# Performance work log

Measured on AMD Instinct MI355X. Metric: run time of the kernel, lower is better.

## Reference

```python
import jax, jax.numpy as jnp
import numpy as np

B, S, D, H, DK = 8, 1024, 1024, 16, 64
DV = D // H  # 64


def setup_inputs() -> dict:
    key = jax.random.key(0)
    ks = jax.random.split(key, 9)
    s = 1.0 / np.sqrt(D)
    return {
        "x": jax.random.normal(ks[0], (B, S, D), dtype=jnp.float32),
        "masks": jnp.ones((B, S), dtype=jnp.int32),
        "Wq": jax.random.normal(ks[1], (D, H * DK), dtype=jnp.float32) * s,
        "bq": jnp.zeros((H * DK,), dtype=jnp.float32),
        "Wk": jax.random.normal(ks[2], (D, H * DK), dtype=jnp.float32) * s,
        "bk": jnp.zeros((H * DK,), dtype=jnp.float32),
        "Wv": jax.random.normal(ks[3], (D, H * DV), dtype=jnp.float32) * s,
        "bv": jnp.zeros((H * DV,), dtype=jnp.float32),
        "Wo": jax.random.normal(ks[4], (H * DV, D), dtype=jnp.float32) * s,
        "bo": jnpp_zeros() if False else jnp.zeros((D,), dtype=jnp.float32),
    }


def reference(x, masks, Wq, bq, Wk, bk, Wv, bv, Wo, bo):
    # projections -> [B, H, S, d]
    q = (x @ Wq + bq).reshape(B, S, H, DK).transpose(0, 2, 1, 3)
    k = (x @ Wk + bk).reshape(B, S, H, DK).transpose(0, 2, 1, 3)
    v = (x @ Wv + bv).reshape(B, S, H, DV).transpose(0, 2, 1, 3)
    # scaled dot-product attention with padding mask
    logits = jnp.einsum('bhqd,bhkd->bhqk', q, k) / jnp.sqrt(jnp.float32(DK))
    mask = masks[:, None, None, :]  # [B,1,1,S]
    logits = jnp.where(mask == 0, jnp.float32(-1e9), logits)
    scores = jax.nn.softmax(logits, axis=-1)
    out = jnp.einsum('bhqk,bhkd->bhqd', scores, v)
    out = out.transpose(0, 2, 1, 3).reshape(B, S, H * DV)
    # output projection; dropout is identity in eval mode
    return out @ Wo + bo
```

## Files before the change

### kernel.cpp

```cpp
#include <hip/hip_runtime.h>
#include <stdint.h>

#define B_ 8
#define S_ 1024
#define D_ 1024
#define H_ 16
#define DK_ 64
#define DV_ 64

typedef __attribute__((ext_vector_type(8))) short short8;
typedef __attribute__((ext_vector_type(4))) float f32x4;

__device__ __forceinline__ unsigned short f2bf(float f) {
  union { float f; unsigned u; } v; v.f = f;
  return (unsigned short)((v.u + 0x7fffu + ((v.u >> 16) & 1u)) >> 16);
}
__device__ __forceinline__ unsigned short f2bf_trunc(float f) {
  union { float f; unsigned u; } v; v.f = f;
  return (unsigned short)(v.u >> 16);
}

__device__ __forceinline__ void ld_lds16(const unsigned short* g, unsigned short* l) {
  __builtin_amdgcn_global_load_lds((const __attribute__((address_space(1))) void*)g,
                                   (__attribute__((address_space(3))) void*)l, 16, 0, 0);
}

__global__ __launch_bounds__(256) void prep_kernel(const float* __restrict__ x,
                                                   unsigned short* __restrict__ xb,
                                                   const float* __restrict__ W0,
                                                   const float* __restrict__ W1,
                                                   const float* __restrict__ W2,
                                                   const float* __restrict__ W3,
                                                   unsigned short* __restrict__ T0,
                                                   unsigned short* __restrict__ T1,
                                                   unsigned short* __restrict__ T2,
                                                   unsigned short* __restrict__ T3) {
  const int z = blockIdx.z;
  if (z >= 4) {
    size_t blk = (size_t)(z - 4) * 256 + blockIdx.y * 16 + blockIdx.x;
    size_t i = (blk * 256 + threadIdx.x) * 4;
    float4 v = *(const float4*)(x + i);
    ushort4 o;
    o.x = f2bf(v.x); o.y = f2bf(v.y); o.z = f2bf(v.z); o.w = f2bf(v.w);
    *(ushort4*)(xb + i) = o;
    return;
  }
  __shared__ __align__(16) unsigned short tl[64][65];
  const float* W; unsigned short* Wt;
  switch (z) {
    case 0: W = W0; Wt = T0; break;
    case 1: W = W1; Wt = T1; break;
    case 2: W = W2; Wt = T2; break;
    default: W = W3; Wt = T3; break;
  }
  const int xx = threadIdx.x & 63;
  const int y4 = threadIdx.x >> 6;
  const int bn = blockIdx.x * 64;
  const int bk = blockIdx.y * 64;
  #pragma unroll
  for (int r = y4; r < 64; r += 4)
    tl[r][xx] = f2bf(W[(size_t)(bk + r) * 1024 + bn + xx]);
  __syncthreads();
  #pragma unroll
  for (int r = y4; r < 64; r += 4)
    Wt[(size_t)(bn + r) * 1024 + bk + xx] = tl[xx][r];
}


struct SJob { const unsigned short* g; unsigned short* l; };

__device__ __forceinline__ void stage128(const unsigned short* __restrict__ G,
                                         unsigned short* __restrict__ L, int t) {
  #pragma unroll
  for (int i = 0; i < 2; i++) {
    int s = i * 512 + t;
    int r = s >> 3, cb = s & 7;
    int c = cb ^ (r & 7);
    ld_lds16(G + (size_t)r * 1024 + c * 8, L + (size_t)s * 8);
  }
}

template <bool SW>
__device__ __forceinline__ f32x4 MM(short8 a, short8 b, f32x4 c) {
  if constexpr (SW) return __builtin_amdgcn_mfma_f32_16x16x32_bf16(b, a, c, 0, 0, 0);
  else              return __builtin_amdgcn_mfma_f32_16x16x32_bf16(a, b, c, 0, 0, 0);
}

template <bool SW, int VM>
__device__ __forceinline__ void ktile2(const unsigned short* __restrict__ As_,
                                       const unsigned short* __restrict__ Bs_,
                                       f32x4 (&acc)[4][4],
                                       SJob a0, SJob a1, SJob b2,
                                       int t, int wm, int wn, int l15, int quad, int l7) {
  const int cb0 = (quad ^ l7) * 8;
  const int cb1 = ((4 | quad) ^ l7) * 8;
  short8 af[4], bf[4];

  #pragma unroll
  for (int mi = 0; mi < 4; mi++)
    af[mi] = *(const short8*)&As_[(wm + mi * 16 + l15) * 64 + cb0];
  #pragma unroll
  for (int ni = 0; ni < 4; ni++)
    bf[ni] = *(const short8*)&Bs_[(wn + ni * 16 + l15) * 64 + cb0];
  if (a0.g) stage128(a0.g, a0.l, t);
  if (a1.g) stage128(a1.g, a1.l, t);
  if (b2.g) stage128(b2.g, b2.l, t);
  __builtin_amdgcn_s_barrier();
  asm volatile("s_waitcnt lgkmcnt(0)" ::: "memory");
  __builtin_amdgcn_s_setprio(1);
  #pragma unroll
  for (int mi = 0; mi < 4; mi++)
    #pragma unroll
    for (int ni = 0; ni < 4; ni++)
      acc[mi][ni] = MM<SW>(af[mi], bf[ni], acc[mi][ni]);
  __builtin_amdgcn_s_setprio(0);
  __builtin_amdgcn_s_barrier();

  #pragma unroll
  for (int mi = 0; mi < 4; mi++)
    af[mi] = *(const short8*)&As_[(wm + mi * 16 + l15) * 64 + cb1];
  #pragma unroll
  for (int ni = 0; ni < 4; ni++)
    bf[ni] = *(const short8*)&Bs_[(wn + ni * 16 + l15) * 64 + cb1];
  __builtin_amdgcn_s_barrier();
  asm volatile("s_waitcnt lgkmcnt(0)" ::: "memory");
  __builtin_amdgcn_s_setprio(1);
  #pragma unroll
  for (int mi = 0; mi < 4; mi++)
    #pragma unroll
    for (int ni = 0; ni < 4; ni++)
      acc[mi][ni] = MM<SW>(af[mi], bf[ni], acc[mi][ni]);
  __builtin_amdgcn_s_setprio(0);
  if constexpr (VM >= 0) {
    if constexpr (VM == 2) asm volatile("s_waitcnt vmcnt(2)" ::: "memory");
    else                   asm volatile("s_waitcnt vmcnt(0)" ::: "memory");
  }
  __builtin_amdgcn_s_barrier();
}

template <bool SW>
__device__ __forceinline__ void gemm_core(const unsigned short* __restrict__ Ag,
                                          const unsigned short* __restrict__ Bg,
                                          unsigned short* __restrict__ Asl,
                                          unsigned short* __restrict__ Bsl,
                                          f32x4 (&acc)[4][4],
                                          int t, int wm, int wn, int l15, int quad, int l7) {
  stage128(Ag, &Asl[0], t);
  stage128(Ag + 128 * 1024, &Asl[8192], t);
  stage128(Bg, &Bsl[0], t);
  stage128(Bg + 64, &Bsl[8192], t);
  asm volatile("s_waitcnt vmcnt(2)" ::: "memory");
  __builtin_amdgcn_s_barrier();

  #pragma unroll 1
  for (int Jb = 0; Jb < 12; Jb += 6) {
    const unsigned short* Agj = Ag + (size_t)Jb * 64;
    const unsigned short* Bgj = Bg + (size_t)Jb * 64;
    ktile2<SW, 2>(&Asl[0], &Bsl[0], acc,
                  SJob{Agj + 64, &Asl[16384]}, SJob{Agj + 64 + 128 * 1024, &Asl[16384 + 8192]},
                  SJob{Bgj + 128, &Bsl[16384]}, t, wm, wn, l15, quad, l7);
    ktile2<SW, 2>(&Asl[16384], &Bsl[8192], acc,
                  SJob{Agj + 128, &Asl[0]}, SJob{Agj + 128 + 128 * 1024, &Asl[8192]},
                  SJob{Bgj + 192, &Bsl[0]}, t, wm, wn, l15, quad, l7);
    ktile2<SW, 2>(&Asl[0], &Bsl[16384], acc,
                  SJob{Agj + 192, &Asl[16384]}, SJob{Agj + 192 + 128 * 1024, &Asl[16384 + 8192]},
                  SJob{Bgj + 256, &Bsl[8192]}, t, wm, wn, l15, quad, l7);
    ktile2<SW, 2>(&Asl[16384], &Bsl[0], acc,
                  SJob{Agj + 256, &Asl[0]}, SJob{Agj + 256 + 128 * 1024, &Asl[8192]},
                  SJob{Bgj + 320, &Bsl[16384]}, t, wm, wn, l15, quad, l7);
    ktile2<SW, 2>(&Asl[0], &Bsl[8192], acc,
                  SJob{Agj + 320, &Asl[16384]}, SJob{Agj + 320 + 128 * 1024, &Asl[16384 + 8192]},
                  SJob{Bgj + 384, &Bsl[0]}, t, wm, wn, l15, quad, l7);
    ktile2<SW, 2>(&Asl[16384], &Bsl[16384], acc,
                  SJob{Agj + 384, &Asl[0]}, SJob{Agj + 384 + 128 * 1024, &Asl[8192]},
                  SJob{Bgj + 448, &Bsl[8192]}, t, wm, wn, l15, quad, l7);
  }
  ktile2<SW, 2>(&Asl[0], &Bsl[0], acc,
                SJob{Ag + 13 * 64, &Asl[16384]}, SJob{Ag + 13 * 64 + 128 * 1024, &Asl[16384 + 8192]},
                SJob{Bg + 14 * 64, &Bsl[16384]}, t, wm, wn, l15, quad, l7);
  ktile2<SW, 2>(&Asl[16384], &Bsl[8192], acc,
                SJob{Ag + 14 * 64, &Asl[0]}, SJob{Ag + 14 * 64 + 128 * 1024, &Asl[8192]},
                SJob{Bg + 15 * 64, &Bsl[0]}, t, wm, wn, l15, quad, l7);
  ktile2<SW, 0>(&Asl[0], &Bsl[16384], acc,
                SJob{Ag + 15 * 64, &Asl[16384]}, SJob{Ag + 15 * 64 + 128 * 1024, &Asl[16384 + 8192]},
                SJob{nullptr, nullptr}, t, wm, wn, l15, quad, l7);
  ktile2<SW, -1>(&Asl[16384], &Bsl[0], acc,
                 SJob{nullptr, nullptr}, SJob{nullptr, nullptr}, SJob{nullptr, nullptr},
                 t, wm, wn, l15, quad, l7);
}

__global__ __launch_bounds__(512, 2) void gemm_qkv8(const unsigned short* __restrict__ A,
                                                    const unsigned short* __restrict__ Bt,
                                                    const float* __restrict__ bq,
                                                    const float* __restrict__ bk,
                                                    const float* __restrict__ bv,
                                                    const int* __restrict__ masks,
                                                    unsigned short* __restrict__ q,
                                                    unsigned short* __restrict__ kk,
                                                    unsigned short* __restrict__ vT) {
  extern __shared__ unsigned short lds[];
  unsigned short* Asl = lds;
  unsigned short* Bsl = lds + 2 * 16384;
  const int t = threadIdx.x;
  const int w = t >> 6, lane = t & 63;
  const int l15 = lane & 15, quad = lane >> 4, l7 = l15 & 7;
  const int bm = blockIdx.y * 256, bn = blockIdx.x * 128;
  const int wm = (w >> 1) * 64, wn = (w & 1) * 64;
  const bool vsec = (blockIdx.x >= 16);
  const unsigned short* Ag = A + (size_t)bm * 1024;
  const unsigned short* Bg = Bt + (size_t)bn * 1024;

  f32x4 acc[4][4] = {};
  if (!vsec) gemm_core<false>(Ag, Bg, Asl, Bsl, acc, t, wm, wn, l15, quad, l7);
  else       gemm_core<true >(Ag, Bg, Asl, Bsl, acc, t, wm, wn, l15, quad, l7);

  if (!vsec) {
    int sec = blockIdx.x >> 3;
    const float* bsel = (sec == 0) ? bq : bk;
    unsigned short* dst = (sec == 0) ? q : kk;
    float scale = (sec == 0) ? 0.180336880f : 1.0f;
    #pragma unroll
    for (int ni = 0; ni < 4; ni++) {
      int c = (bn & 1023) + wn + ni * 16 + l15;
      float bvv = bsel[c];
      int hh = c >> 6, d = c & 63;
      #pragma unroll
      for (int mi = 0; mi < 4; mi++) {
        int row0 = bm + wm + mi * 16 + quad * 4;
        #pragma unroll
        for (int r = 0; r < 4; r++) {
          int row = row0 + r;
          int b = row >> 10, s = row & 1023;
          dst[(((size_t)(b * H_ + hh)) * S_ + s) * DK_ + d] = f2bf((acc[mi][ni][r] + bvv) * scale);
        }
      }
    }
  } else {
    #pragma unroll
    for (int ni = 0; ni < 4; ni++) {
      int cbase = (bn & 1023) + wn + ni * 16;
      #pragma unroll
      for (int mi = 0; mi < 4; mi++) {
        int row = bm + wm + mi * 16 + l15;
        int b = row >> 10, s = row & 1023;
        float mf = (masks[b * S_ + s] != 0) ? 1.0f : 0.0f;
        #pragma unroll
        for (int r = 0; r < 4; r++) {
          int c = cbase + quad * 4 + r;
          int hh = c >> 6, d = c & 63;
          vT[(((size_t)(b * H_ + hh)) * DV_ + d) * S_ + s] = f2bf((acc[mi][ni][r] + bv[c]) * mf);
        }
      }
    }
  }
}

__global__ __launch_bounds__(512, 2) void gemm_out8(const unsigned short* __restrict__ A,
                                                    const unsigned short* __restrict__ Bt,
                                                    const float* __restrict__ bias,
                                                    float* __restrict__ Cout) {
  extern __shared__ unsigned short lds[];
  unsigned short* Asl = lds;
  unsigned short* Bsl = lds + 2 * 16384;
  const int t = threadIdx.x;
  const int w = t >> 6, lane = t & 63;
  const int l15 = lane & 15, quad = lane >> 4, l7 = l15 & 7;
  const int bm = blockIdx.y * 256, bn = blockIdx.x * 128;
  const int wm = (w >> 1) * 64, wn = (w & 1) * 64;
  const unsigned short* Ag = A + (size_t)bm * 1024;
  const unsigned short* Bg = Bt + (size_t)bn * 1024;

  f32x4 acc[4][4] = {};
  gemm_core<false>(Ag, Bg, Asl, Bsl, acc, t, wm, wn, l15, quad, l7);

  #pragma unroll
  for (int ni = 0; ni < 4; ni++) {
    int col = bn + wn + ni * 16 + l15;
    float bvv = bias[col];
    #pragma unroll
    for (int mi = 0; mi < 4; mi++) {
      int row0 = bm + wm + mi * 16 + quad * 4;
      #pragma unroll
      for (int r = 0; r < 4; r++)
        Cout[(size_t)(row0 + r) * 1024 + col] = acc[mi][ni][r] + bvv;
    }
  }
}

#define PLD 72
#define VROWS 65
__global__ __launch_bounds__(256) void attn_kernel(const unsigned short* __restrict__ Q,
                                                   const unsigned short* __restrict__ Kb,
                                                   const unsigned short* __restrict__ Vt,
                                                   const int* __restrict__ masks,
                                                   unsigned short* __restrict__ O) {
  __shared__ __align__(16) unsigned short Pl[128 * PLD];
  __shared__ __align__(16) unsigned short Ks[2 * 64 * 64];
  __shared__ __align__(16) unsigned short Vs[(2 * VROWS + 15) * 64];
  const int t = threadIdx.x;
  const int wave = t >> 6, lane = t & 63;
  const int l15 = lane & 15, quad = lane >> 4;
  const int l7 = l15 & 7;
  const int bh = blockIdx.x;
  const int qt = blockIdx.y;
  const int b = bh >> 4, h = bh & 15;

  const unsigned short* Qg = Q + ((size_t)bh * S_ + qt * 128) * DK_;
  const unsigned short* Kg = Kb + (size_t)bh * S_ * DK_;
  const unsigned short* Vg = Vt + (size_t)bh * DV_ * S_;
  const int wslot = (t & ~63);

  int mv[4];
  #pragma unroll
  for (int j = 0; j < 4; j++)
    mv[j] = masks[b * S_ + (j * 4 + wave) * 64 + lane];

  short8 aq[2][2];
  #pragma unroll
  for (int mb = 0; mb < 2; mb++)
    #pragma unroll
    for (int kf = 0; kf < 2; kf++)
      aq[mb][kf] = *(const short8*)(Qg + (size_t)(wave * 32 + mb * 16 + l15) * 64 + kf * 32 + quad * 8);

  auto stage = [&](int kt, int buf) {
    const unsigned short* Kt = Kg + (size_t)kt * 64 * DK_;
    unsigned short* Kd = &Ks[buf * 4096];
    unsigned short* Vd = &Vs[buf * (VROWS * 64)];
    #pragma unroll
    for (int i = 0; i < 2; i++) {
      int p = i * 256 + t;
      int rk = p >> 3, ck = (p & 7) ^ (rk & 7);
      ld_lds16(Kt + (size_t)rk * DK_ + ck * 8, &Kd[(i * 256 + wslot) * 8]);
      ld_lds16(Vg + (size_t)rk * S_ + kt * 64 + ck * 8, &Vd[(i * 256 + wslot) * 8]);
    }
    if (wave == (kt & 3))
      Vd[64 * 64 + lane] = (mv[kt >> 2] != 0) ? (unsigned short)0x3F80 : (unsigned short)0;
  };

  f32x4 o_acc[2][5] = {};

  stage(0, 0);
  __syncthreads();

  #pragma unroll 2
  for (int kt = 0; kt < 16; kt++) {
    const int cur = kt & 1;
    if (kt < 15) stage(kt + 1, cur ^ 1);
    const unsigned short* Kc = &Ks[cur * 4096];
    const unsigned short* Vc = &Vs[cur * (VROWS * 64)];

    f32x4 sc[2][4];
    #pragma unroll
    for (int n = 0; n < 4; n++) {
      short8 bk0 = *(const short8*)&Kc[(n * 16 + l15) * 64 + (quad ^ l7) * 8];
      short8 bk1 = *(const short8*)&Kc[(n * 16 + l15) * 64 + ((4 + quad) ^ l7) * 8];
      #pragma unroll
      for (int mb = 0; mb < 2; mb++) {
        f32x4 c = {};
        c = __builtin_amdgcn_mfma_f32_16x16x32_bf16(bk0, aq[mb][0], c, 0, 0, 0);
        c = __builtin_amdgcn_mfma_f32_16x16x32_bf16(bk1, aq[mb][1], c, 0, 0, 0);
        sc[mb][n] = c;
      }
    }
    #pragma unroll
    for (int mb = 0; mb < 2; mb++)
      #pragma unroll
      for (int n = 0; n < 4; n++) {
        ushort4 pk;
        pk.x = f2bf_trunc(__builtin_amdgcn_exp2f(sc[mb][n][0]));
        pk.y = f2bf_trunc(__builtin_amdgcn_exp2f(sc[mb][n][1]));
        pk.z = f2bf_trunc(__builtin_amdgcn_exp2f(sc[mb][n][2]));
        pk.w = f2bf_trunc(__builtin_amdgcn_exp2f(sc[mb][n][3]));
        *(ushort4*)&Pl[(wave * 32 + mb * 16 + l15) * PLD + n * 16 + quad * 4] = pk;
      }
    #pragma unroll
    for (int kf = 0; kf < 2; kf++) {
      short8 ap[2];
      #pragma unroll
      for (int mb = 0; mb < 2; mb++)
        ap[mb] = *(const short8*)&Pl[(wave * 32 + mb * 16 + l15) * PLD + kf * 32 + quad * 8];
      #pragma unroll
      for (int n = 0; n < 5; n++) {
        short8 bv = *(const short8*)&Vc[(n * 16 + l15) * 64 + ((kf * 4 + quad) ^ l7) * 8];
        #pragma unroll
        for (int mb = 0; mb < 2; mb++)
          o_acc[mb][n] = __builtin_amdgcn_mfma_f32_16x16x32_bf16(ap[mb], bv, o_acc[mb][n], 0, 0, 0);
      }
    }
    __syncthreads();
  }

  #pragma unroll
  for (int mb = 0; mb < 2; mb++)
    #pragma unroll
    for (int r = 0; r < 4; r++) {
      float l = __shfl(o_acc[mb][4][r], lane & 48, 64);
      float inv = __builtin_amdgcn_rcpf(l);
      int qrow = qt * 128 + wave * 32 + mb * 16 + quad * 4 + r;
      #pragma unroll
      for (int n = 0; n < 4; n++) {
        int col = h * 64 + n * 16 + l15;
        O[((size_t)b * S_ + qrow) * D_ + col] = f2bf(o_acc[mb][n][r] * inv);
      }
    }
}

extern "C" void kernel_launch(void* const* d_in, const int* in_sizes, int n_in,
                              void* d_out, int out_size, void* d_ws, size_t ws_size,
                              hipStream_t stream) {
  (void)in_sizes; (void)n_in; (void)out_size; (void)ws_size;
  const float* x  = (const float*)d_in[0];
  const int* masks = (const int*)d_in[1];
  const float* Wq = (const float*)d_in[2];
  const float* bq = (const float*)d_in[3];
  const float* Wk = (const float*)d_in[4];
  const float* bk = (const float*)d_in[5];
  const float* Wv = (const float*)d_in[6];
  const float* bv = (const float*)d_in[7];
  const float* Wo = (const float*)d_in[8];
  const float* bo = (const float*)d_in[9];

  char* p = (char*)d_ws;
  unsigned short* xb    = (unsigned short*)p; p += (size_t)8192 * 1024 * 2;
  unsigned short* WqkvT = (unsigned short*)p; p += (size_t)3072 * 1024 * 2;
  unsigned short* WoT   = (unsigned short*)p; p += (size_t)1024 * 1024 * 2;
  unsigned short* q     = (unsigned short*)p; p += (size_t)8192 * 1024 * 2;
  unsigned short* kk    = (unsigned short*)p; p += (size_t)8192 * 1024 * 2;
  unsigned short* vT    = (unsigned short*)p; p += (size_t)8192 * 1024 * 2;
  unsigned short* at    = (unsigned short*)p; p += (size_t)8192 * 1024 * 2;

  static bool attr_done = false;
  if (!attr_done) {
    hipFuncSetAttribute((const void*)gemm_qkv8, hipFuncAttributeMaxDynamicSharedMemorySize, 114688);
    hipFuncSetAttribute((const void*)gemm_out8, hipFuncAttributeMaxDynamicSharedMemorySize, 114688);
    attr_done = true;
  }

  prep_kernel<<<dim3(16, 16, 36), 256, 0, stream>>>(
      x, xb, Wq, Wk, Wv, Wo,
      WqkvT, WqkvT + (size_t)1024 * 1024, WqkvT + (size_t)2048 * 1024, WoT);
  gemm_qkv8<<<dim3(24, 32), 512, 114688, stream>>>(xb, WqkvT, bq, bk, bv, masks, q, kk, vT);
  attn_kernel<<<dim3(128, 8), 256, 0, stream>>>(q, kk, vT, masks, at);
  gemm_out8<<<dim3(8, 32), 512, 114688, stream>>>(at, WoT, bo, (float*)d_out);
}
```

Before: 251.2 us.

## Triple-buffer GEMM LDS pipeline and remap blocks across XCDs

Restructures the shared GEMM core from double to triple LDS buffering, prefetching two k-tiles ahead and waiting on vmcnt(6) instead of vmcnt(2). The B-tile load is issued after the first half-tile of MFMAs rather than together with the A loads. Both GEMM kernels also remap linear block IDs so that consecutive blocks land on different XCDs, aiming for better L2 locality. Dynamic LDS rises to 144 KB per block, which constrains occupancy.

```diff
diff --git a/kernel.cpp b/kernel.cpp
--- a/kernel.cpp
+++ b/kernel.cpp
@@ -104,6 +104,23 @@
     bf[ni] = *(const short8*)&Bs_[(wn + ni * 16 + l15) * 64 + cb0];
   if (a0.g) stage128(a0.g, a0.l, t);
   if (a1.g) stage128(a1.g, a1.l, t);
+  __builtin_amdgcn_s_barrier();
+  asm volatile("s_waitcnt lgkmcnt(0)" ::: "memory");
+  __builtin_amdgcn_s_setprio(1);
+  #pragma unroll
+  for (int mi = 0; mi < 4; mi++)
+    #pragma unroll
+    for (int ni = 0; ni < 4; ni++)
+      acc[mi][ni] = MM<SW>(af[mi], bf[ni], acc[mi][ni]);
+  __builtin_amdgcn_s_setprio(0);
+  __builtin_amdgcn_s_barrier();
+
+  #pragma unroll
+  for (int mi = 0; mi < 4; mi++)
+    af[mi] = *(const short8*)&As_[(wm + mi * 16 + l15) * 64 + cb1];
+  #pragma unroll
+  for (int ni = 0; ni < 4; ni++)
+    bf[ni] = *(const short8*)&Bs_[(wn + ni * 16 + l15) * 64 + cb1];
   if (b2.g) stage128(b2.g, b2.l, t);
   __builtin_amdgcn_s_barrier();
   asm volatile("s_waitcnt lgkmcnt(0)" ::: "memory");
@@ -114,27 +131,8 @@
     for (int ni = 0; ni < 4; ni++)
       acc[mi][ni] = MM<SW>(af[mi], bf[ni], acc[mi][ni]);
   __builtin_amdgcn_s_setprio(0);
-  __builtin_amdgcn_s_barrier();
-
-  #pragma unroll
-  for (int mi = 0; mi < 4; mi++)
-    af[mi] = *(const short8*)&As_[(wm + mi * 16 + l15) * 64 + cb1];
-  #pragma unroll
-  for (int ni = 0; ni < 4; ni++)
-    bf[ni] = *(const short8*)&Bs_[(wn + ni * 16 + l15) * 64 + cb1];
-  __builtin_amdgcn_s_barrier();
-  asm volatile("s_waitcnt lgkmcnt(0)" ::: "memory");
-  __builtin_amdgcn_s_setprio(1);
-  #pragma unroll
-  for (int mi = 0; mi < 4; mi++)
-    #pragma unroll
-    for (int ni = 0; ni < 4; ni++)
-      acc[mi][ni] = MM<SW>(af[mi], bf[ni], acc[mi][ni]);
-  __builtin_amdgcn_s_setprio(0);
-  if constexpr (VM >= 0) {
-    if constexpr (VM == 2) asm volatile("s_waitcnt vmcnt(2)" ::: "memory");
-    else                   asm volatile("s_waitcnt vmcnt(0)" ::: "memory");
-  }
+  if constexpr (VM == 6) asm volatile("s_waitcnt vmcnt(6)" ::: "memory");
+  if constexpr (VM == 0) asm volatile("s_waitcnt vmcnt(0)" ::: "memory");
   __builtin_amdgcn_s_barrier();
 }
 
@@ -145,46 +143,46 @@
                                           unsigned short* __restrict__ Bsl,
                                           f32x4 (&acc)[4][4],
                                           int t, int wm, int wn, int l15, int quad, int l7) {
-  stage128(Ag, &Asl[0], t);
-  stage128(Ag + 128 * 1024, &Asl[8192], t);
-  stage128(Bg, &Bsl[0], t);
-  stage128(Bg + 64, &Bsl[8192], t);
-  asm volatile("s_waitcnt vmcnt(2)" ::: "memory");
+  unsigned short* A0 = Asl;
+  unsigned short* A1 = Asl + 16384;
+  unsigned short* A2 = Asl + 32768;
+  unsigned short* Bs0 = Bsl;
+  unsigned short* Bs1 = Bsl + 8192;
+  unsigned short* Bs2 = Bsl + 16384;
+
+  stage128(Ag,                 A0, t);
+  stage128(Ag + 128 * 1024,    A0 + 8192, t);
+  stage128(Bg,                 Bs0, t);
+  stage128(Ag + 64,                A1, t);
+  stage128(Ag + 64 + 128 * 1024,   A1 + 8192, t);
+  stage128(Bg + 64,                Bs1, t);
+  asm volatile("s_waitcnt vmcnt(6)" ::: "memory");
   __builtin_amdgcn_s_barrier();
 
   #pragma unroll 1
-  for (int Jb = 0; Jb < 12; Jb += 6) {
-    const unsigned short* Agj = Ag + (size_t)Jb * 64;
-    const unsigned short* Bgj = Bg + (size_t)Jb * 64;
-    ktile2<SW, 2>(&Asl[0], &Bsl[0], acc,
-                  SJob{Agj + 64, &Asl[16384]}, SJob{Agj + 64 + 128 * 1024, &Asl[16384 + 8192]},
-                  SJob{Bgj + 128, &Bsl[16384]}, t, wm, wn, l15, quad, l7);
-    ktile2<SW, 2>(&Asl[16384], &Bsl[8192], acc,
-                  SJob{Agj + 128, &Asl[0]}, SJob{Agj + 128 + 128 * 1024, &Asl[8192]},
-                  SJob{Bgj + 192, &Bsl[0]}, t, wm, wn, l15, quad, l7);
-    ktile2<SW, 2>(&Asl[0], &Bsl[16384], acc,
-                  SJob{Agj + 192, &Asl[16384]}, SJob{Agj + 192 + 128 * 1024, &Asl[16384 + 8192]},
-                  SJob{Bgj + 256, &Bsl[8192]}, t, wm, wn, l15, quad, l7);
-    ktile2<SW, 2>(&Asl[16384], &Bsl[0], acc,
-                  SJob{Agj + 256, &Asl[0]}, SJob{Agj + 256 + 128 * 1024, &Asl[8192]},
-                  SJob{Bgj + 320, &Bsl[16384]}, t, wm, wn, l15, quad, l7);
-    ktile2<SW, 2>(&Asl[0], &Bsl[8192], acc,
-                  SJob{Agj + 320, &Asl[16384]}, SJob{Agj + 320 + 128 * 1024, &Asl[16384 + 8192]},
-                  SJob{Bgj + 384, &Bsl[0]}, t, wm, wn, l15, quad, l7);
-    ktile2<SW, 2>(&Asl[16384], &Bsl[16384], acc,
-                  SJob{Agj + 384, &Asl[0]}, SJob{Agj + 384 + 128 * 1024, &Asl[8192]},
-                  SJob{Bgj + 448, &Bsl[8192]}, t, wm, wn, l15, quad, l7);
-  }
-  ktile2<SW, 2>(&Asl[0], &Bsl[0], acc,
-                SJob{Ag + 13 * 64, &Asl[16384]}, SJob{Ag + 13 * 64 + 128 * 1024, &Asl[16384 + 8192]},
-                SJob{Bg + 14 * 64, &Bsl[16384]}, t, wm, wn, l15, quad, l7);
-  ktile2<SW, 2>(&Asl[16384], &Bsl[8192], acc,
-                SJob{Ag + 14 * 64, &Asl[0]}, SJob{Ag + 14 * 64 + 128 * 1024, &Asl[8192]},
-                SJob{Bg + 15 * 64, &Bsl[0]}, t, wm, wn, l15, quad, l7);
-  ktile2<SW, 0>(&Asl[0], &Bsl[16384], acc,
-                SJob{Ag + 15 * 64, &Asl[16384]}, SJob{Ag + 15 * 64 + 128 * 1024, &Asl[16384 + 8192]},
-                SJob{nullptr, nullptr}, t, wm, wn, l15, quad, l7);
-  ktile2<SW, -1>(&Asl[16384], &Bsl[0], acc,
+  for (int J = 0; J < 12; J += 3) {
+    const unsigned short* Aj = Ag + (size_t)J * 64;
+    const unsigned short* Bj = Bg + (size_t)J * 64;
+    ktile2<SW, 6>(A0, Bs0, acc,
+                  SJob{Aj + 2 * 64, A2}, SJob{Aj + 2 * 64 + 128 * 1024, A2 + 8192},
+                  SJob{Bj + 2 * 64, Bs2}, t, wm, wn, l15, quad, l7);
+    ktile2<SW, 6>(A1, Bs1, acc,
+                  SJob{Aj + 3 * 64, A0}, SJob{Aj + 3 * 64 + 128 * 1024, A0 + 8192},
+                  SJob{Bj + 3 * 64, Bs0}, t, wm, wn, l15, quad, l7);
+    ktile2<SW, 6>(A2, Bs2, acc,
+                  SJob{Aj + 4 * 64, A1}, SJob{Aj + 4 * 64 + 128 * 1024, A1 + 8192},
+                  SJob{Bj + 4 * 64, Bs1}, t, wm, wn, l15, quad, l7);
+  }
+  ktile2<SW, 6>(A0, Bs0, acc,
+                SJob{Ag + 14 * 64, A2}, SJob{Ag + 14 * 64 + 128 * 1024, A2 + 8192},
+                SJob{Bg + 14 * 64, Bs2}, t, wm, wn, l15, quad, l7);
+  ktile2<SW, 6>(A1, Bs1, acc,
+                SJob{Ag + 15 * 64, A0}, SJob{Ag + 15 * 64 + 128 * 1024, A0 + 8192},
+                SJob{Bg + 15 * 64, Bs0}, t, wm, wn, l15, quad, l7);
+  ktile2<SW, 0>(A2, Bs2, acc,
+                SJob{nullptr, nullptr}, SJob{nullptr, nullptr}, SJob{nullptr, nullptr},
+                t, wm, wn, l15, quad, l7);
+  ktile2<SW, -1>(A0, Bs0, acc,
                  SJob{nullptr, nullptr}, SJob{nullptr, nullptr}, SJob{nullptr, nullptr},
                  t, wm, wn, l15, quad, l7);
 }
@@ -200,13 +198,16 @@
                                                     unsigned short* __restrict__ vT) {
   extern __shared__ unsigned short lds[];
   unsigned short* Asl = lds;
-  unsigned short* Bsl = lds + 2 * 16384;
+  unsigned short* Bsl = lds + 3 * 16384;
   const int t = threadIdx.x;
   const int w = t >> 6, lane = t & 63;
   const int l15 = lane & 15, quad = lane >> 4, l7 = l15 & 7;
-  const int bm = blockIdx.y * 256, bn = blockIdx.x * 128;
+  const int lin = blockIdx.y * 24 + blockIdx.x;
+  const int lin2 = (lin & 7) * 96 + (lin >> 3);
+  const int bxi = lin2 % 24, byi = lin2 / 24;
+  const int bm = byi * 256, bn = bxi * 128;
   const int wm = (w >> 1) * 64, wn = (w & 1) * 64;
-  const bool vsec = (blockIdx.x >= 16);
+  const bool vsec = (bxi >= 16);
   const unsigned short* Ag = A + (size_t)bm * 1024;
   const unsigned short* Bg = Bt + (size_t)bn * 1024;
 
@@ -215,7 +216,7 @@
   else       gemm_core<true >(Ag, Bg, Asl, Bsl, acc, t, wm, wn, l15, quad, l7);
 
   if (!vsec) {
-    int sec = blockIdx.x >> 3;
+    int sec = bxi >> 3;
     const float* bsel = (sec == 0) ? bq : bk;
     unsigned short* dst = (sec == 0) ? q : kk;
     float scale = (sec == 0) ? 0.180336880f : 1.0f;
@@ -261,11 +262,14 @@
                                                     float* __restrict__ Cout) {
   extern __shared__ unsigned short lds[];
   unsigned short* Asl = lds;
-  unsigned short* Bsl = lds + 2 * 16384;
+  unsigned short* Bsl = lds + 3 * 16384;
   const int t = threadIdx.x;
   const int w = t >> 6, lane = t & 63;
   const int l15 = lane & 15, quad = lane >> 4, l7 = l15 & 7;
-  const int bm = blockIdx.y * 256, bn = blockIdx.x * 128;
+  const int lin = blockIdx.y * 8 + blockIdx.x;
+  const int lin2 = (lin & 7) * 32 + (lin >> 3);
+  const int bxi = lin2 % 8, byi = lin2 / 8;
+  const int bm = byi * 256, bn = bxi * 128;
   const int wm = (w >> 1) * 64, wn = (w & 1) * 64;
   const unsigned short* Ag = A + (size_t)bm * 1024;
   const unsigned short* Bg = Bt + (size_t)bn * 1024;
@@ -431,15 +435,15 @@
 
   static bool attr_done = false;
   if (!attr_done) {
-    hipFuncSetAttribute((const void*)gemm_qkv8, hipFuncAttributeMaxDynamicSharedMemorySize, 114688);
-    hipFuncSetAttribute((const void*)gemm_out8, hipFuncAttributeMaxDynamicSharedMemorySize, 114688);
+    hipFuncSetAttribute((const void*)gemm_qkv8, hipFuncAttributeMaxDynamicSharedMemorySize, 147456);
+    hipFuncSetAttribute((const void*)gemm_out8, hipFuncAttributeMaxDynamicSharedMemorySize, 147456);
     attr_done = true;
   }
 
   prep_kernel<<<dim3(16, 16, 36), 256, 0, stream>>>(
       x, xb, Wq, Wk, Wv, Wo,
       WqkvT, WqkvT + (size_t)1024 * 1024, WqkvT + (size_t)2048 * 1024, WoT);
-  gemm_qkv8<<<dim3(24, 32), 512, 114688, stream>>>(xb, WqkvT, bq, bk, bv, masks, q, kk, vT);
+  gemm_qkv8<<<dim3(24, 32), 512, 147456, stream>>>(xb, WqkvT, bq, bk, bv, masks, q, kk, vT);
   attn_kernel<<<dim3(128, 8), 256, 0, stream>>>(q, kk, vT, masks, at);
-  gemm_out8<<<dim3(8, 32), 512, 114688, stream>>>(at, WoT, bo, (float*)d_out);
-}
+  gemm_out8<<<dim3(8, 32), 512, 147456, stream>>>(at, WoT, bo, (float*)d_out);
+}
```

Result: no change. 249.3 us (-0.7%).
